# Performance work log

Measured on AMD Instinct MI355X. Metric: run time of the kernel, lower is better.

The kernel has to match this reference:

```python
import jax, jax.numpy as jnp
import numpy as np

N, E, D, H, L = 20000, 100000, 768, 8, 3
DH = D // H
WSCALE = 0.02  # small init so exp() in attention stays finite


def setup_inputs() -> dict:
    key = jax.random.key(0)
    ks = jax.random.split(key, 16)
    inp = {
        'x': jax.random.normal(ks[0], (N, D), jnp.float32),
        'edge_attr': jax.random.normal(ks[1], (E, D), jnp.float32),
        'Wck': jax.random.normal(ks[2], (L, 2 * D, D), jnp.float32) * WSCALE,
        'bck': jnp.zeros((L, D), jnp.float32),
        'Wq': jax.random.normal(ks[3], (L, D, D), jnp.float32) * WSCALE,
        'bq': jnp.zeros((L, D), jnp.float32),
        'Wv': jax.random.normal(ks[4], (L, D, D), jnp.float32) * WSCALE,
        'bv': jnp.zeros((L, D), jnp.float32),
        'Waw': jax.random.normal(ks[5], (L, H, H), jnp.float32) * WSCALE,
        'baw': jnp.zeros((L, H), jnp.float32),
        'Wc': jax.random.normal(ks[6], (L, D, D), jnp.float32) * WSCALE,
        'bc': jnp.zeros((L, D), jnp.float32),
        'Wlx': jax.random.normal(ks[7], (L, D, D), jnp.float32) * WSCALE,
        'blx': jnp.zeros((L, D), jnp.float32),
        'Wla1': jax.random.normal(ks[8], (L, 2 * D, D), jnp.float32) * WSCALE,
        'bla1': jnp.zeros((L, D), jnp.float32),
        'Wla2': jax.random.normal(ks[9], (L, D, 2), jnp.float32) * WSCALE,
        'bla2': jnp.zeros((L, 2), jnp.float32),
        'edge_index': jax.random.randint(ks[10], (2, E), 0, N, jnp.int64),
    }
    return inp


def _gnn_layer(x, edge_attr, src, dst, Wck, bck, Wq, bq, Wv, bv, Waw, baw,
               Wc, bc, Wlx, blx, Wla1, bla1, Wla2, bla2):
    n = x.shape[0]
    # per-edge query (target node) and key (edge_attr || source node)
    q = x[dst] @ Wq + bq                                        # [E, D]
    k = jnp.concatenate([edge_attr, x[src]], axis=1) @ Wck + bck  # [E, D]
    qh = q.reshape(-1, H, DH)
    kh = k.reshape(-1, H, DH)
    aw = jnp.einsum('ehd,ehd->eh', qh, kh) / jnp.sqrt(jnp.float32(D))  # [E, H]
    a = jnp.exp(jax.nn.leaky_relu(aw, 0.2) @ Waw + baw)          # [E, H]
    # GAT-style softmax normalization over incoming edges of each target node
    sc = jax.ops.segment_sum(a, dst, num_segments=n)             # [N, H]
    ad = sc[dst]
    ad = jnp.where(ad == 0, jnp.float32(1), ad)
    att = (a / ad)[:, :, None]                                   # [E, H, 1]
    # weighted message from source nodes, scattered to targets
    v = (x[src] @ Wv + bv).reshape(-1, H, DH)                    # [E, H, DH]
    msg = (att * v).reshape(-1, D) @ Wc + bc                     # [E, D]
    h = jax.ops.segment_sum(msg, dst, num_segments=n)            # [N, D]
    # sgnn gated residual combine
    lx = x @ Wlx + blx
    z = jax.nn.leaky_relu(jnp.concatenate([lx, h], axis=1) @ Wla1 + bla1, 0.2) @ Wla2 + bla2
    la = jax.nn.softmax(z, axis=1)                               # [N, 2]
    return x * la[:, 0:1] + h * la[:, 1:2]


def reference(x, edge_attr, Wck, bck, Wq, bq, Wv, bv, Waw, baw, Wc, bc,
              Wlx, blx, Wla1, bla1, Wla2, bla2, edge_index):
    src = edge_index[0]
    dst = edge_index[1]
    for l in range(L):
        x = _gnn_layer(x, edge_attr, src, dst,
                       Wck[l], bck[l], Wq[l], bq[l], Wv[l], bv[l],
                       Waw[l], baw[l], Wc[l], bc[l], Wlx[l], blx[l],
                       Wla1[l], bla1[l], Wla2[l], bla2[l])
    return x
```

## Files before the change

### kernel.cpp

```cpp
#include <hip/hip_runtime.h>
#include <hip/hip_bf16.h>
#include <math.h>

#define DD 768
#define HH 8
#define DHH 96
#define NL 3
#define NN 20000
#define EE 100000

typedef __attribute__((ext_vector_type(8))) __bf16 bf16x8;
typedef __attribute__((ext_vector_type(4))) float f32x4;
typedef __attribute__((ext_vector_type(8))) unsigned short u16x8;

__host__ __device__ static inline int imin(int a, int b) { return a < b ? a : b; }

__device__ inline float b2f(unsigned short u) {
    union { unsigned int v; float f; } x; x.v = ((unsigned int)u) << 16; return x.f;
}
__device__ inline unsigned short f2b_rne(float f) {
    union { float f; unsigned int v; } x; x.f = f;
    unsigned int v = x.v;
    return (unsigned short)((v + 0x7FFFu + ((v >> 16) & 1u)) >> 16);
}
__device__ inline void b2f2(unsigned int u, float& lo, float& hi) {
    union { unsigned int v; float f; } x;
    x.v = u << 16; lo = x.f;
    x.v = u & 0xffff0000u; hi = x.f;
}
__device__ inline unsigned int packbf(float a, float b) {
    return (unsigned int)f2b_rne(a) | ((unsigned int)f2b_rne(b) << 16);
}

__global__ void deg_kernel(const int* __restrict__ dst, int* __restrict__ cnt)
{
    int i = blockIdx.x * 256 + threadIdx.x;
    if (i < EE) atomicAdd(&cnt[dst[i]], 1);
}

__global__ __launch_bounds__(256)
void scan_kernel(const int* __restrict__ deg, int* __restrict__ rowptr, int* __restrict__ cursor)
{
    __shared__ int part[256];
    int t = threadIdx.x;
    const int per = (NN + 255) / 256;
    int lo = t * per, hi = imin(NN, lo + per);
    int s = 0;
    for (int i = lo; i < hi; i++) s += deg[i];
    part[t] = s;
    __syncthreads();
    if (t == 0) {
        int acc = 0;
        for (int i = 0; i < 256; i++) { int v = part[i]; part[i] = acc; acc += v; }
        rowptr[NN] = acc;
    }
    __syncthreads();
    int run = part[t];
    for (int i = lo; i < hi; i++) {
        rowptr[i] = run; cursor[i] = run;
        run += deg[i];
    }
}

__global__ void fill_perm(const int* __restrict__ src, const int* __restrict__ dst,
                          int* __restrict__ cursor, int* __restrict__ perm,
                          int* __restrict__ src_s)
{
    int e = blockIdx.x * 256 + threadIdx.x;
    if (e >= EE) return;
    int d = dst[e];
    int pos = atomicAdd(&cursor[d], 1);
    perm[pos] = e;
    src_s[pos] = src[e];
}

__global__ void degf_kernel(const int* __restrict__ rowptr, float* __restrict__ degf)
{
    int n = blockIdx.x * 256 + threadIdx.x;
    if (n < NN) degf[n] = (float)(rowptr[n + 1] - rowptr[n]);
}

__global__ void f2b_kernel(const float* __restrict__ in, unsigned short* __restrict__ out, int n8)
{
    int i = blockIdx.x * 256 + threadIdx.x;
    if (i >= n8) return;
    const float4* p = reinterpret_cast<const float4*>(in + (size_t)i * 8);
    float4 a = p[0], b = p[1];
    u16x8 o;
    o[0] = f2b_rne(a.x); o[1] = f2b_rne(a.y); o[2] = f2b_rne(a.z); o[3] = f2b_rne(a.w);
    o[4] = f2b_rne(b.x); o[5] = f2b_rne(b.y); o[6] = f2b_rne(b.z); o[7] = f2b_rne(b.w);
    *reinterpret_cast<u16x8*>(out + (size_t)i * 8) = o;
}

__global__ void f2b_gather(const float* __restrict__ in, const int* __restrict__ perm,
                           unsigned short* __restrict__ out)
{
    int i = blockIdx.x * 256 + threadIdx.x;
    if (i >= EE * 96) return;
    int m = i / 96;
    int d8 = (i % 96) * 8;
    int row = perm[m];
    const float4* p = reinterpret_cast<const float4*>(in + (size_t)row * DD + d8);
    float4 a = p[0], b = p[1];
    u16x8 o;
    o[0] = f2b_rne(a.x); o[1] = f2b_rne(a.y); o[2] = f2b_rne(a.z); o[3] = f2b_rne(a.w);
    o[4] = f2b_rne(b.x); o[5] = f2b_rne(b.y); o[6] = f2b_rne(b.z); o[7] = f2b_rne(b.w);
    *reinterpret_cast<u16x8*>(out + (size_t)m * DD + d8) = o;
}

__global__ void transpose_w(const float* __restrict__ W, unsigned short* __restrict__ Wt,
                            int Kin, int out_ld, int out_off,
                            size_t strideW, size_t strideWt)
{
    __shared__ float tile[32][33];
    int z = blockIdx.z;
    W  += (size_t)z * strideW;
    Wt += (size_t)z * strideWt;
    int kb = blockIdx.x * 32, nb = blockIdx.y * 32;
    int tx = threadIdx.x & 31, ty = threadIdx.x >> 5;
#pragma unroll
    for (int i = 0; i < 32; i += 8)
        tile[ty + i][tx] = W[(size_t)(kb + ty + i) * DD + nb + tx];
    __syncthreads();
#pragma unroll
    for (int i = 0; i < 32; i += 8)
        Wt[(size_t)(nb + ty + i) * out_ld + out_off + kb + tx] = f2b_rne(tile[tx][ty + i]);
}

__global__ void biasf_kernel(const float* __restrict__ blx, const float* __restrict__ Wla1,
                             const float* __restrict__ bla1, float* __restrict__ bf)
{
    int l = blockIdx.y;
    const float* blxl  = blx  + (size_t)l * DD;
    const float* Wla1l = Wla1 + (size_t)l * 2 * DD * DD;
    const float* bla1l = bla1 + (size_t)l * DD;
    float* bfl = bf + (size_t)l * DD;
    int n = blockIdx.x * 256 + threadIdx.x;
    if (n >= DD) return;
    float s = bla1l[n];
    for (int k = 0; k < DD; k++) s += blxl[k] * Wla1l[(size_t)k * DD + n];
    bfl[n] = s;
}

__global__ void biasqkv_kernel(const float* __restrict__ bq, const float* __restrict__ bv,
                               float* __restrict__ bqkv)
{
    int l = blockIdx.y;
    int i = blockIdx.x * 256 + threadIdx.x;
    if (i >= 3 * DD) return;
    float v = 0.f;
    if (i < DD) v = bq[(size_t)l * DD + i];
    else if (i >= 2 * DD) v = bv[(size_t)l * DD + i - 2 * DD];
    bqkv[(size_t)l * 3 * DD + i] = v;
}

__global__ __launch_bounds__(512, 4)
void gemm_mfma(const unsigned short* __restrict__ A0,
               const unsigned short* __restrict__ A1,
               const unsigned short* __restrict__ Wt,
               const float* __restrict__ bias,
               const float* __restrict__ rowscale,
               float* __restrict__ C32,
               unsigned short* __restrict__ C16,
               int M, int K, int Nw,
               size_t bsA, size_t bsW, size_t bsC)
{
    __shared__ __align__(16) char smem[49152];
    char* As = smem;
    char* Bs = smem + 32768;
    const int z = blockIdx.z;
    A0 += (size_t)z * bsA;
    Wt += (size_t)z * bsW;
    if (C32) C32 += (size_t)z * bsC;
    if (C16) C16 += (size_t)z * bsC;
    const int t = threadIdx.x;
    const int l = t & 63;
    const int w = t >> 6;
    const int wm = w & 3, wn = w >> 2;

    const int gx = gridDim.x;
    const int nwg = gx * gridDim.y;
    const int lin = blockIdx.y * gx + blockIdx.x;
    const int xcd = lin & 7, pos = lin >> 3;
    const int q8 = nwg >> 3, r8 = nwg & 7;
    const int base = (xcd < r8) ? xcd * (q8 + 1) : r8 * (q8 + 1) + (xcd - r8) * q8;
    const int swz = base + pos;
    const int bn = swz % gx, bm = swz / gx;

    const int srow = t >> 3;
    const int ssrc = ((t & 7) ^ (srow & 7)) * 8;

    const int lane_r = l & 15;
    const int lane_k = l >> 4;

    f32x4 acc[4][4];
#pragma unroll
    for (int m = 0; m < 4; m++)
#pragma unroll
        for (int n = 0; n < 4; n++) acc[m][n] = (f32x4){0.f, 0.f, 0.f, 0.f};

    for (int k0 = 0; k0 < K; k0 += 64) {
        const unsigned short* Ap; int kbase;
        if (k0 < DD) { Ap = A0; kbase = k0; }
        else         { Ap = A1; kbase = k0 - DD; }
#pragma unroll
        for (int i = 0; i < 4; i++) {
            int grow = bm * 256 + i * 64 + srow;
            char* ldstA = As + ((i * 64 + w * 8) << 7);
            if (grow < M) {
                const unsigned short* g = Ap + (size_t)grow * DD + kbase + ssrc;
                __builtin_amdgcn_global_load_lds(
                    (const __attribute__((address_space(1))) void*)g,
                    (__attribute__((address_space(3))) void*)ldstA, 16, 0, 0);
            }
        }
#pragma unroll
        for (int i = 0; i < 2; i++) {
            int gn = bn * 128 + i * 64 + srow;
            const unsigned short* gB = Wt + (size_t)gn * K + k0 + ssrc;
            char* ldstB = Bs + ((i * 64 + w * 8) << 7);
            __builtin_amdgcn_global_load_lds(
                (const __attribute__((address_space(1))) void*)gB,
                (__attribute__((address_space(3))) void*)ldstB, 16, 0, 0);
        }
        __syncthreads();
#pragma unroll
        for (int kk = 0; kk < 2; kk++) {
            bf16x8 af[4], bfr[4];
#pragma unroll
            for (int m = 0; m < 4; m++) {
                int r = wm * 64 + m * 16 + lane_r;
                int slot = (kk * 4 + lane_k) ^ (r & 7);
                af[m] = *reinterpret_cast<const bf16x8*>(As + r * 128 + slot * 16);
            }
#pragma unroll
            for (int n = 0; n < 4; n++) {
                int r = wn * 64 + n * 16 + lane_r;
                int slot = (kk * 4 + lane_k) ^ (r & 7);
                bfr[n] = *reinterpret_cast<const bf16x8*>(Bs + r * 128 + slot * 16);
            }
#pragma unroll
            for (int m = 0; m < 4; m++)
#pragma unroll
                for (int n = 0; n < 4; n++)
                    acc[m][n] = __builtin_amdgcn_mfma_f32_16x16x32_bf16(
                        af[m], bfr[n], acc[m][n], 0, 0, 0);
        }
        __syncthreads();
    }

    if (C32) {
#pragma unroll
        for (int n = 0; n < 4; n++) {
            int col = bn * 128 + wn * 64 + n * 16 + lane_r;
            float badd = bias ? bias[col] : 0.f;
#pragma unroll
            for (int m = 0; m < 4; m++) {
#pragma unroll
                for (int j = 0; j < 4; j++) {
                    int r = bm * 256 + wm * 64 + m * 16 + lane_k * 4 + j;
                    if (r < M) {
                        float bs = rowscale ? rowscale[r] : 1.f;
                        C32[(size_t)r * Nw + col] = acc[m][n][j] + badd * bs;
                    }
                }
            }
        }
    }
    if (C16) {
        unsigned short* cs = (unsigned short*)smem;
#pragma unroll
        for (int half = 0; half < 2; half++) {
            __syncthreads();
            if ((wm >> 1) == half) {
#pragma unroll
                for (int n = 0; n < 4; n++) {
                    int lcol = wn * 64 + n * 16 + lane_r;
                    float badd = bias ? bias[bn * 128 + lcol] : 0.f;
#pragma unroll
                    for (int m = 0; m < 4; m++) {
#pragma unroll
                        for (int j = 0; j < 4; j++) {
                            int lr = (wm & 1) * 64 + m * 16 + lane_k * 4 + j;
                            int r = bm * 256 + half * 128 + lr;
                            float bs = rowscale ? (r < M ? rowscale[r] : 0.f) : 1.f;
                            cs[lr * 136 + lcol] = f2b_rne(acc[m][n][j] + badd * bs);
                        }
                    }
                }
            }
            __syncthreads();
            int rr = t >> 2, qd = (t & 3) * 32;
            int grow = bm * 256 + half * 128 + rr;
            if (grow < M) {
                u16x8* dst = reinterpret_cast<u16x8*>(C16 + (size_t)grow * Nw + bn * 128 + qd);
                const u16x8* s = reinterpret_cast<const u16x8*>(cs + rr * 136 + qd);
                dst[0] = s[0];
                dst[1] = s[1];
                dst[2] = s[2];
                dst[3] = s[3];
            }
        }
    }
}

__global__ __launch_bounds__(128)
void edge_fused(const unsigned short* __restrict__ kea,
                const unsigned short* __restrict__ qkv,
                const float* __restrict__ Waw, const float* __restrict__ baw,
                const int* __restrict__ rowptr, const int* __restrict__ src_s,
                unsigned short* __restrict__ agg)
{
    __shared__ float awsh[HH];
    __shared__ float WawS[HH * HH];
    __shared__ float bawS[HH];
    const int n = blockIdx.x;
    const int t = threadIdx.x;
    const int d0 = t * 6;
    const int h = t >> 4;
    if (t < HH * HH) WawS[t] = Waw[t];
    if (t < HH) bawS[t] = baw[t];
    const int jlo = rowptr[n], jhi = rowptr[n + 1];
    const unsigned int* qr = reinterpret_cast<const unsigned int*>(qkv + (size_t)n * (3 * DD) + d0);
    float q[6];
    b2f2(qr[0], q[0], q[1]); b2f2(qr[1], q[2], q[3]); b2f2(qr[2], q[4], q[5]);
    float acc[6] = {0.f, 0.f, 0.f, 0.f, 0.f, 0.f};
    float sa = 0.f;
    constexpr float rs = 0.03608439182435161f;
    __syncthreads();
    for (int j = jlo; j < jhi; j++) {
        int s = src_s[j];
        const unsigned int* ke = reinterpret_cast<const unsigned int*>(kea + (size_t)j * DD + d0);
        const unsigned int* kr = reinterpret_cast<const unsigned int*>(qkv + (size_t)s * (3 * DD) + DD + d0);
        const unsigned int* vr = reinterpret_cast<const unsigned int*>(qkv + (size_t)s * (3 * DD) + 2 * DD + d0);
        float part = 0.f;
        float ka, kb2, va, vb;
#pragma unroll
        for (int c = 0; c < 3; c++) {
            b2f2(ke[c], ka, kb2);
            b2f2(kr[c], va, vb);
            part = fmaf(q[2 * c], ka + va, part);
            part = fmaf(q[2 * c + 1], kb2 + vb, part);
        }
        part += __shfl_xor(part, 1);
        part += __shfl_xor(part, 2);
        part += __shfl_xor(part, 4);
        part += __shfl_xor(part, 8);
        if ((t & 15) == 0) awsh[h] = part;
        __syncthreads();
        float zz = bawS[h];
#pragma unroll
        for (int h2 = 0; h2 < HH; h2++) {
            float aw = awsh[h2] * rs;
            float tt = aw > 0.f ? aw : 0.2f * aw;
            zz = fmaf(tt, WawS[h2 * HH + h], zz);
        }
        float a = expf(zz);
        sa += a;
        float v0, v1;
#pragma unroll
        for (int c = 0; c < 3; c++) {
            b2f2(vr[c], v0, v1);
            acc[2 * c]     = fmaf(a, v0, acc[2 * c]);
            acc[2 * c + 1] = fmaf(a, v1, acc[2 * c + 1]);
        }
        __syncthreads();
    }
    float inv = (sa == 0.f) ? 1.f : 1.f / sa;
    unsigned int* ag = reinterpret_cast<unsigned int*>(agg + (size_t)n * DD + d0);
    ag[0] = packbf(acc[0] * inv, acc[1] * inv);
    ag[1] = packbf(acc[2] * inv, acc[3] * inv);
    ag[2] = packbf(acc[4] * inv, acc[5] * inv);
}

__global__ __launch_bounds__(256)
void combine_kernel(const unsigned short* __restrict__ g, const float* __restrict__ Wla2,
                    const float* __restrict__ bla2, unsigned short* __restrict__ x16,
                    const unsigned short* __restrict__ h, float* __restrict__ outf, int Nn)
{
    int w = threadIdx.x >> 6;
    int lane = threadIdx.x & 63;
    int n = blockIdx.x * 4 + w;
    if (n >= Nn) return;
    float z0 = 0.f, z1 = 0.f;
#pragma unroll
    for (int p = 0; p < 3; p++) {
        int d = p * 256 + lane * 4;
        const unsigned short* gp = g + (size_t)n * DD + d;
#pragma unroll
        for (int j = 0; j < 4; j++) {
            float gv = b2f(gp[j]);
            float tt = gv > 0.f ? gv : 0.2f * gv;
            z0 = fmaf(tt, Wla2[(d + j) * 2 + 0], z0);
            z1 = fmaf(tt, Wla2[(d + j) * 2 + 1], z1);
        }
    }
#pragma unroll
    for (int off = 32; off > 0; off >>= 1) {
        z0 += __shfl_xor(z0, off);
        z1 += __shfl_xor(z1, off);
    }
    z0 += bla2[0]; z1 += bla2[1];
    float mx = fmaxf(z0, z1);
    float e0v = expf(z0 - mx), e1v = expf(z1 - mx);
    float inv = 1.f / (e0v + e1v);
    float la0 = e0v * inv, la1 = e1v * inv;
#pragma unroll
    for (int p = 0; p < 3; p++) {
        int d = p * 256 + lane * 4;
        unsigned short* xp = x16 + (size_t)n * DD + d;
        const unsigned short* hp = h + (size_t)n * DD + d;
        float o[4];
#pragma unroll
        for (int j = 0; j < 4; j++)
            o[j] = b2f(xp[j]) * la0 + b2f(hp[j]) * la1;
#pragma unroll
        for (int j = 0; j < 4; j++) xp[j] = f2b_rne(o[j]);
        if (outf) {
            float4 ov = make_float4(o[0], o[1], o[2], o[3]);
            *reinterpret_cast<float4*>((float*)outf + (size_t)n * DD + d) = ov;
        }
    }
}

extern "C" void kernel_launch(void* const* d_in, const int* in_sizes, int n_in,
                              void* d_out, int out_size, void* d_ws, size_t ws_size,
                              hipStream_t stream)
{
    const int N = NN, E = EE;
    const float* x_in      = (const float*)d_in[0];
    const float* edge_attr = (const float*)d_in[1];
    const float* Wck = (const float*)d_in[2];
    const float* bck = (const float*)d_in[3];
    const float* Wq  = (const float*)d_in[4];
    const float* bq  = (const float*)d_in[5];
    const float* Wv  = (const float*)d_in[6];
    const float* bv  = (const float*)d_in[7];
    const float* Waw = (const float*)d_in[8];
    const float* baw = (const float*)d_in[9];
    const float* Wc  = (const float*)d_in[10];
    const float* bc  = (const float*)d_in[11];
    const float* Wlx = (const float*)d_in[12];
    const float* blx = (const float*)d_in[13];
    const float* Wla1 = (const float*)d_in[14];
    const float* bla1 = (const float*)d_in[15];
    const float* Wla2 = (const float*)d_in[16];
    const float* bla2 = (const float*)d_in[17];
    const int* eidx = (const int*)d_in[18];
    const int* srcp = eidx;
    const int* dstp = eidx + E;

    const size_t DDDD = (size_t)DD * DD;
    float* p = (float*)d_ws;
    const size_t NB = (size_t)N * DD;
    float* degf  = p; p += N;
    float* wfx32 = p; p += NL * DDDD;
    float* bfbuf = p; p += NL * DD;
    float* bqkvb = p; p += NL * 3 * DD;
    int* rowptr = (int*)p;
    int* cursor = rowptr + (N + 1);
    int* perm   = cursor + N;
    int* src_s  = perm + E;
    p += (size_t)(2 * N + 1 + 2 * E + 63) / 64 * 64;
    unsigned short* xb16  = (unsigned short*)p; p += NB / 2;
    unsigned short* hb16  = (unsigned short*)p; p += NB / 2;
    unsigned short* agg16 = (unsigned short*)p; p += NB / 2;
    unsigned short* qkv16 = (unsigned short*)p; p += 3 * NB / 2;
    unsigned short* ea16  = (unsigned short*)p; p += (size_t)E * DD / 2;
    unsigned short* kea16 = (unsigned short*)p; p += (size_t)E * DD / 2;
    unsigned short* gb16  = qkv16;
    unsigned short* wqkvt  = (unsigned short*)p; p += NL * 3 * DDDD / 2;
    unsigned short* wcktopt= (unsigned short*)p; p += NL * DDDD / 2;
    unsigned short* wct    = (unsigned short*)p; p += NL * DDDD / 2;
    unsigned short* wla1tt = (unsigned short*)p; p += NL * DDDD / 2;
    unsigned short* wst3   = (unsigned short*)p; p += NL * 2 * DDDD / 2;
    unsigned short* wlx16  = (unsigned short*)p; p += NL * DDDD / 2;

    hipMemsetAsync(cursor, 0, N * sizeof(int), stream);
    deg_kernel<<<(E + 255) / 256, 256, 0, stream>>>(dstp, cursor);
    scan_kernel<<<1, 256, 0, stream>>>(cursor, rowptr, cursor);
    fill_perm<<<(E + 255) / 256, 256, 0, stream>>>(srcp, dstp, cursor, perm, src_s);
    degf_kernel<<<(N + 255) / 256, 256, 0, stream>>>(rowptr, degf);
    f2b_gather<<<(E * 96 + 255) / 256, 256, 0, stream>>>(edge_attr, perm, ea16);
    f2b_kernel<<<(N * 96 + 255) / 256, 256, 0, stream>>>(x_in, xb16, N * 96);

    dim3 gt3(DD / 32, DD / 32, NL);
    transpose_w<<<gt3, 256, 0, stream>>>(Wq, wqkvt, DD, DD, 0, DDDD, 3 * DDDD);
    transpose_w<<<gt3, 256, 0, stream>>>(Wck + DDDD, wqkvt + DDDD, DD, DD, 0, 2 * DDDD, 3 * DDDD);
    transpose_w<<<gt3, 256, 0, stream>>>(Wv, wqkvt + 2 * DDDD, DD, DD, 0, DDDD, 3 * DDDD);
    transpose_w<<<gt3, 256, 0, stream>>>(Wck, wcktopt, DD, DD, 0, 2 * DDDD, DDDD);
    transpose_w<<<gt3, 256, 0, stream>>>(Wc, wct, DD, DD, 0, DDDD, DDDD);
    transpose_w<<<gt3, 256, 0, stream>>>(Wla1, wla1tt, DD, DD, 0, 2 * DDDD, DDDD);
    transpose_w<<<gt3, 256, 0, stream>>>(Wla1 + DDDD, wst3, DD, 2 * DD, DD, 2 * DDDD, 2 * DDDD);
    f2b_kernel<<<(NL * DD * 96 + 255) / 256, 256, 0, stream>>>(Wlx, wlx16, NL * DD * 96);
    gemm_mfma<<<dim3(6, 3, NL), 512, 0, stream>>>(wlx16, nullptr, wla1tt, nullptr, nullptr,
                                                  wfx32, nullptr, DD, DD, DD,
                                                  DDDD, DDDD, DDDD);
    transpose_w<<<gt3, 256, 0, stream>>>(wfx32, wst3, DD, 2 * DD, 0, DDDD, 2 * DDDD);
    biasf_kernel<<<dim3(3, NL), 256, 0, stream>>>(blx, Wla1, bla1, bfbuf);
    biasqkv_kernel<<<dim3(9, NL), 256, 0, stream>>>(bq, bv, bqkvb);

    for (int l = 0; l < NL; l++) {
        const float* bck_l = bck + (size_t)l * DD;
        const float* Waw_l = Waw + (size_t)l * HH * HH;
        const float* baw_l = baw + (size_t)l * HH;
        const float* bc_l  = bc  + (size_t)l * DD;
        const float* Wla2_l = Wla2 + (size_t)l * DD * 2;
        const float* bla2_l = bla2 + (size_t)l * 2;

        gemm_mfma<<<dim3(18, (N + 255) / 256), 512, 0, stream>>>(
            xb16, nullptr, wqkvt + (size_t)l * 3 * DDDD, bqkvb + (size_t)l * 3 * DD,
            nullptr, nullptr, qkv16, N, DD, 3 * DD, 0, 0, 0);
        gemm_mfma<<<dim3(6, (E + 255) / 256), 512, 0, stream>>>(
            ea16, nullptr, wcktopt + (size_t)l * DDDD, bck_l,
            nullptr, nullptr, kea16, E, DD, DD, 0, 0, 0);
        edge_fused<<<N, 128, 0, stream>>>(kea16, qkv16, Waw_l, baw_l, rowptr, src_s, agg16);
        gemm_mfma<<<dim3(6, (N + 255) / 256), 512, 0, stream>>>(
            agg16, nullptr, wct + (size_t)l * DDDD, bc_l,
            degf, nullptr, hb16, N, DD, DD, 0, 0, 0);
        gemm_mfma<<<dim3(6, (N + 255) / 256), 512, 0, stream>>>(
            xb16, hb16, wst3 + (size_t)l * 2 * DDDD, bfbuf + (size_t)l * DD,
            nullptr, nullptr, gb16, N, 2 * DD, DD, 0, 0, 0);
        combine_kernel<<<(N + 3) / 4, 256, 0, stream>>>(
            gb16, Wla2_l, bla2_l, xb16, hb16,
            (l == NL - 1) ? (float*)d_out : nullptr, N);
    }
}
```

Before: 1.776 ms.

## Double-buffer GEMM LDS tiles and write bf16 epilogue in one pass

Splits the GEMM main loop into a double-buffered pipeline: the next K tile is loaded into a second LDS buffer with global_load_lds while MFMAs run on the current one, so only one barrier is needed per iteration. It raises MFMA wave priority with s_setprio around the compute block. The larger 96KB LDS buffer also lets the bf16 output staging cover the whole 256-row tile in one pass instead of two halves. The cost is double the LDS per block, with the occupancy hint lowered from 4 to 2 blocks per CU, which may reduce latency hiding.

```diff
diff --git a/kernel.cpp b/kernel.cpp
--- a/kernel.cpp
+++ b/kernel.cpp
@@ -154,7 +154,7 @@
     bqkv[(size_t)l * 3 * DD + i] = v;
 }
 
-__global__ __launch_bounds__(512, 4)
+__global__ __launch_bounds__(512, 2)
 void gemm_mfma(const unsigned short* __restrict__ A0,
                const unsigned short* __restrict__ A1,
                const unsigned short* __restrict__ Wt,
@@ -165,9 +165,7 @@
                int M, int K, int Nw,
                size_t bsA, size_t bsW, size_t bsC)
 {
-    __shared__ __align__(16) char smem[49152];
-    char* As = smem;
-    char* Bs = smem + 32768;
+    __shared__ __align__(16) char smem[98304];
     const int z = blockIdx.z;
     A0 += (size_t)z * bsA;
     Wt += (size_t)z * bsW;
@@ -193,13 +191,9 @@
     const int lane_r = l & 15;
     const int lane_k = l >> 4;
 
-    f32x4 acc[4][4];
-#pragma unroll
-    for (int m = 0; m < 4; m++)
-#pragma unroll
-        for (int n = 0; n < 4; n++) acc[m][n] = (f32x4){0.f, 0.f, 0.f, 0.f};
-
-    for (int k0 = 0; k0 < K; k0 += 64) {
+    auto STAGE = [&](int buf, int k0) {
+        char* As = smem + buf * 49152;
+        char* Bs = As + 32768;
         const unsigned short* Ap; int kbase;
         if (k0 < DD) { Ap = A0; kbase = k0; }
         else         { Ap = A1; kbase = k0 - DD; }
@@ -223,7 +217,23 @@
                 (const __attribute__((address_space(1))) void*)gB,
                 (__attribute__((address_space(3))) void*)ldstB, 16, 0, 0);
         }
-        __syncthreads();
+    };
+
+    f32x4 acc[4][4];
+#pragma unroll
+    for (int m = 0; m < 4; m++)
+#pragma unroll
+        for (int n = 0; n < 4; n++) acc[m][n] = (f32x4){0.f, 0.f, 0.f, 0.f};
+
+    const int nt = K >> 6;
+    STAGE(0, 0);
+    __syncthreads();
+    int cur = 0;
+    for (int tt = 0; tt < nt; tt++) {
+        if (tt + 1 < nt) STAGE(cur ^ 1, (tt + 1) << 6);
+        char* As = smem + cur * 49152;
+        char* Bs = As + 32768;
+        __builtin_amdgcn_s_setprio(1);
 #pragma unroll
         for (int kk = 0; kk < 2; kk++) {
             bf16x8 af[4], bfr[4];
@@ -246,7 +256,9 @@
                     acc[m][n] = __builtin_amdgcn_mfma_f32_16x16x32_bf16(
                         af[m], bfr[n], acc[m][n], 0, 0, 0);
         }
+        __builtin_amdgcn_s_setprio(0);
         __syncthreads();
+        cur ^= 1;
     }
 
     if (C32) {
@@ -270,36 +282,28 @@
     if (C16) {
         unsigned short* cs = (unsigned short*)smem;
 #pragma unroll
-        for (int half = 0; half < 2; half++) {
-            __syncthreads();
-            if ((wm >> 1) == half) {
-#pragma unroll
-                for (int n = 0; n < 4; n++) {
-                    int lcol = wn * 64 + n * 16 + lane_r;
-                    float badd = bias ? bias[bn * 128 + lcol] : 0.f;
-#pragma unroll
-                    for (int m = 0; m < 4; m++) {
-#pragma unroll
-                        for (int j = 0; j < 4; j++) {
-                            int lr = (wm & 1) * 64 + m * 16 + lane_k * 4 + j;
-                            int r = bm * 256 + half * 128 + lr;
-                            float bs = rowscale ? (r < M ? rowscale[r] : 0.f) : 1.f;
-                            cs[lr * 136 + lcol] = f2b_rne(acc[m][n][j] + badd * bs);
-                        }
-                    }
+        for (int n = 0; n < 4; n++) {
+            int lcol = wn * 64 + n * 16 + lane_r;
+            float badd = bias ? bias[bn * 128 + lcol] : 0.f;
+#pragma unroll
+            for (int m = 0; m < 4; m++) {
+#pragma unroll
+                for (int j = 0; j < 4; j++) {
+                    int lr = wm * 64 + m * 16 + lane_k * 4 + j;
+                    int r = bm * 256 + lr;
+                    float bs = rowscale ? (r < M ? rowscale[r] : 0.f) : 1.f;
+                    cs[lr * 136 + lcol] = f2b_rne(acc[m][n][j] + badd * bs);
                 }
             }
-            __syncthreads();
-            int rr = t >> 2, qd = (t & 3) * 32;
-            int grow = bm * 256 + half * 128 + rr;
-            if (grow < M) {
-                u16x8* dst = reinterpret_cast<u16x8*>(C16 + (size_t)grow * Nw + bn * 128 + qd);
-                const u16x8* s = reinterpret_cast<const u16x8*>(cs + rr * 136 + qd);
-                dst[0] = s[0];
-                dst[1] = s[1];
-                dst[2] = s[2];
-                dst[3] = s[3];
-            }
+        }
+        __syncthreads();
+        int rr = t >> 1, half = t & 1;
+        int grow = bm * 256 + rr;
+        if (grow < M) {
+            u16x8* dst = reinterpret_cast<u16x8*>(C16 + (size_t)grow * Nw + bn * 128 + half * 64);
+            const u16x8* s = reinterpret_cast<const u16x8*>(cs + rr * 136 + half * 64);
+#pragma unroll
+            for (int c = 0; c < 8; c++) dst[c] = s[c];
         }
     }
 }
```

Measured after the change: 1.996 ms. 12.4% more time.
